# Kernel tuning notes

Hardware: AMD Instinct MI355X
Metric: run time of the kernel (lower is better)

Reference implementation:

```python
import jax, jax.numpy as jnp
import numpy as np

D_MODEL = 1024
N_HEADS = 16
D_FF = 4096
EPS = 1e-5


def setup_inputs() -> dict:
    key = jax.random.key(0)
    ks = jax.random.split(key, 16)
    s = 1.0 / np.sqrt(D_MODEL)
    x = jax.random.normal(ks[0], (4, 2048, D_MODEL), dtype=jnp.float32)
    Wq = jax.random.normal(ks[1], (D_MODEL, D_MODEL), jnp.float32) * s
    bq = jnp.zeros((D_MODEL,), jnp.float32)
    Wk = jax.random.normal(ks[2], (D_MODEL, D_MODEL), jnp.float32) * s
    bk = jnp.zeros((D_MODEL,), jnp.float32)
    Wv = jax.random.normal(ks[3], (D_MODEL, D_MODEL), jnp.float32) * s
    bv = jnp.zeros((D_MODEL,), jnp.float32)
    Wo = jax.random.normal(ks[4], (D_MODEL, D_MODEL), jnp.float32) * s
    bo = jnp.zeros((D_MODEL,), jnp.float32)
    W1 = jax.random.normal(ks[5], (D_MODEL, D_FF), jnp.float32) * s
    b1 = jnp.zeros((D_FF,), jnp.float32)
    W2 = jax.random.normal(ks[6], (D_FF, D_MODEL), jnp.float32) * (1.0 / np.sqrt(D_FF))
    b2 = jnp.zeros((D_MODEL,), jnp.float32)
    g1 = jnp.ones((D_MODEL,), jnp.float32)
    beta1 = jnp.zeros((D_MODEL,), jnp.float32)
    g2 = jnp.ones((D_MODEL,), jnp.float32)
    beta2 = jnp.zeros((D_MODEL,), jnp.float32)
    return {"x": x, "Wq": Wq, "bq": bq, "Wk": Wk, "bk": bk, "Wv": Wv, "bv": bv,
            "Wo": Wo, "bo": bo, "W1": W1, "b1": b1, "W2": W2, "b2": b2,
            "g1": g1, "beta1": beta1, "g2": g2, "beta2": beta2}


def _layernorm(x, g, b):
    mu = jnp.mean(x, axis=-1, keepdims=True)
    var = jnp.mean(jnp.square(x - mu), axis=-1, keepdims=True)
    return (x - mu) * jax.lax.rsqrt(var + EPS) * g + b


def reference(x, Wq, bq, Wk, bk, Wv, bv, Wo, bo, W1, b1, W2, b2, g1, beta1, g2, beta2):
    B, S, D = x.shape
    H, dk = N_HEADS, D // N_HEADS
    # QKV projections -> [B, H, S, dk]
    q = (x @ Wq + bq).reshape(B, S, H, dk).transpose(0, 2, 1, 3)
    k = (x @ Wk + bk).reshape(B, S, H, dk).transpose(0, 2, 1, 3)
    v = (x @ Wv + bv).reshape(B, S, H, dk).transpose(0, 2, 1, 3)
    scores = jnp.einsum('bhqd,bhkd->bhqk', q, k) / np.sqrt(dk)  # [B,H,S,S]
    attn = jax.nn.softmax(scores, axis=-1)
    out = jnp.einsum('bhqk,bhkd->bhqd', attn, v)
    out = out.transpose(0, 2, 1, 3).reshape(B, S, D) @ Wo + bo
    x2 = _layernorm(x + out, g1, beta1)
    ff = jax.nn.relu(x2 @ W1 + b1) @ W2 + b2
    return _layernorm(x2 + ff, g2, beta2)
```

## Files before the change

kernel.cpp:

```cpp
#include <hip/hip_runtime.h>
#include <math.h>
#include <stdint.h>


#define D_MODEL 1024
#define N_HEADS 16
#define DKH     64
#define D_FF    4096
#define BATCH   4
#define SEQ     2048
#define NTOK    (BATCH * SEQ)
#define LN_EPS  1e-5f
#define QKV_LD  3072
#define QSCALE  0.18033688011112042f

typedef unsigned short u16;
typedef __attribute__((ext_vector_type(8))) short bf16x8;
typedef __attribute__((ext_vector_type(4))) float f32x4;
typedef __attribute__((ext_vector_type(16))) float f32x16;

__device__ __forceinline__ u16 f2bf(float f) {
    union { float f; uint32_t u; } c; c.f = f;
    return (u16)((c.u + 0x7FFFu + ((c.u >> 16) & 1u)) >> 16);
}
__device__ __forceinline__ float bf2f(u16 h) {
    union { uint32_t u; float f; } c; c.u = ((uint32_t)h) << 16;
    return c.f;
}

__device__ __forceinline__ void gload16(const u16* g, u16* lds) {
    __builtin_amdgcn_global_load_lds(
        (const __attribute__((address_space(1))) uint32_t*)g,
        (__attribute__((address_space(3))) uint32_t*)(uintptr_t)lds,
        16, 0, 0);
}

__device__ __forceinline__ void store_out(float* p, float v) { *p = v; }
__device__ __forceinline__ void store_out(u16* p, float v)   { *p = f2bf(v); }

template <int MODE, typename OutT>
__global__ __launch_bounds__(512) void gemm_pipe_kernel(
    const u16* __restrict__ A, const u16* __restrict__ Bt,
    const float* __restrict__ bias, const float* __restrict__ bias2,
    const float* __restrict__ bias3, OutT* __restrict__ C,
    int M, int N, int K)
{
    __shared__ u16 lds[3 * 8192 + 2 * 16384];

    const int tid  = threadIdx.x;
    const int wave = tid >> 6;
    const int lane = tid & 63;
    const int lo   = lane & 15;
    const int hi   = lane >> 4;
    const int wr   = wave >> 2;
    const int wc   = wave & 3;

    const int gx  = gridDim.x;
    const int nwg = gx * gridDim.y;
    int bid = blockIdx.y * gx + blockIdx.x;
    bid = (bid & 7) * (nwg >> 3) + (bid >> 3);
    const int m0 = (bid / gx) << 7;
    const int n0 = (bid % gx) << 8;
    const int NT = K >> 6;

    const int srow = lane >> 3;
    const int schk = (lane & 7) ^ srow;
    const u16* AgS = A  + (size_t)(m0 + wave * 16 + srow) * K + schk * 8;
    const u16* BgS = Bt + (size_t)(n0 + wave * 32 + srow) * K + schk * 8;
    u16* AdS = lds + wave * 1024;
    u16* BdS = lds + 24576 + wave * 2048;

    auto stageA = [&](int kt, int buf) {
        const u16* g = AgS + kt * 64;
        u16* d = AdS + buf * 8192;
#pragma unroll
        for (int q = 0; q < 2; ++q)
            gload16(g + (size_t)q * 8 * K, d + q * 512);
    };
    auto stageB = [&](int kt, int buf) {
        const u16* g = BgS + kt * 64;
        u16* d = BdS + buf * 16384;
#pragma unroll
        for (int q = 0; q < 4; ++q)
            gload16(g + (size_t)q * 8 * K, d + q * 512);
    };

    f32x4 acc[4][4];
#pragma unroll
    for (int i = 0; i < 4; ++i)
#pragma unroll
        for (int j = 0; j < 4; ++j)
#pragma unroll
            for (int r = 0; r < 4; ++r) acc[i][j][r] = 0.f;

    stageA(0, 0);
    stageB(0, 0);
    stageA(1, 1);
    __builtin_amdgcn_sched_barrier(0);
    asm volatile("s_waitcnt vmcnt(2)" ::: "memory");
    __builtin_amdgcn_s_barrier();
    __builtin_amdgcn_sched_barrier(0);

    for (int t = 0; t < NT; ++t) {
        int tb = t + 1; if (tb >= NT) tb = 0;
        int ta = t + 2; if (ta >= NT) ta -= NT;
        stageB(tb, (t + 1) & 1);
        stageA(ta, (t + 2) % 3);

        const u16* Ab = lds + (t % 3) * 8192;
        const u16* Bb = lds + 24576 + (t & 1) * 16384;
#pragma unroll
        for (int ks = 0; ks < 2; ++ks) {
            bf16x8 a[4], b[4];
#pragma unroll
            for (int i = 0; i < 4; ++i) {
                const int ar = wr * 64 + i * 16 + lo;
                a[i] = *(const bf16x8*)&Ab[ar * 64 + (((ks * 4 + hi) ^ (ar & 7)) << 3)];
                const int br = wc * 64 + i * 16 + lo;
                b[i] = *(const bf16x8*)&Bb[br * 64 + (((ks * 4 + hi) ^ (br & 7)) << 3)];
            }
            __builtin_amdgcn_s_setprio(1);
#pragma unroll
            for (int i = 0; i < 4; ++i)
#pragma unroll
                for (int j = 0; j < 4; ++j)
                    acc[i][j] = __builtin_amdgcn_mfma_f32_16x16x32_bf16(
                                    a[i], b[j], acc[i][j], 0, 0, 0);
            __builtin_amdgcn_s_setprio(0);
        }
        __builtin_amdgcn_sched_barrier(0);
        asm volatile("s_waitcnt vmcnt(2)" ::: "memory");
        __builtin_amdgcn_s_barrier();
        __builtin_amdgcn_sched_barrier(0);
    }

    const int crow0 = m0 + wr * 64 + hi * 4;
    const int ccol0 = n0 + wc * 64 + lo;
#pragma unroll
    for (int j = 0; j < 4; ++j) {
        const int col = ccol0 + j * 16;
        float bj;
        float sc = 1.0f;
        if (MODE == 2) {
            bj = (col < 1024) ? bias[col]
               : (col < 2048) ? bias2[col - 1024] : bias3[col - 2048];
            if (col < 1024) sc = QSCALE;
        } else {
            bj = bias[col];
        }
#pragma unroll
        for (int i = 0; i < 4; ++i)
#pragma unroll
            for (int r = 0; r < 4; ++r) {
                float v = acc[i][j][r] + bj;
                if (MODE == 1) v = fmaxf(v, 0.f);
                if (MODE == 2) v *= sc;
                store_out(&C[(size_t)(crow0 + i * 16 + r) * N + col], v);
            }
    }
}

__global__ __launch_bounds__(256, 4) void attn_mfma_kernel(
    const u16* __restrict__ QKV, u16* __restrict__ O)
{
    __shared__ u16 Klds[2][64 * 64];
    __shared__ u16 Vlds[2][64 * 64];

    const int tid  = threadIdx.x;
    const int wave = tid >> 6;
    const int lane = tid & 63;
    const int l31  = lane & 31;
    const int hi5  = lane >> 5;
    const int b    = blockIdx.x >> 4;
    const int h    = blockIdx.x & 15;
    const int q0   = blockIdx.y * 128 + wave * 32;
    const size_t rowb = (size_t)b * SEQ * QKV_LD + (size_t)h * DKH;
    const u16* Qg = QKV + rowb;
    const u16* Kg = QKV + rowb + 1024;
    const u16* Vg = QKV + rowb + 2048;

    bf16x8 qf[4];
#pragma unroll
    for (int f = 0; f < 4; ++f)
        qf[f] = *(const bf16x8*)&Qg[(size_t)(q0 + l31) * QKV_LD + 16 * f + 8 * hi5];

    f32x16 oacc[2];
#pragma unroll
    for (int g = 0; g < 2; ++g)
#pragma unroll
        for (int r = 0; r < 16; ++r) oacc[g][r] = 0.f;
    float mrun = -1e30f, lrun = 0.f;

    const int krow = wave * 8 + (lane >> 3);
    const int kchk = ((lane & 7) ^ (lane >> 3)) << 3;

    const int vdk0 = (tid & 15) * 4;
    const int vkv  = (tid >> 4) * 4;
    const int vchk = vkv >> 3;
    const int vsub = vkv & 7;

    alignas(8) u16 e[4][4];

    auto stageK = [&](int kv0, int buf) {
        u16* kdst = &Klds[buf][wave * 512];
        gload16(Kg + (size_t)(kv0 + krow) * QKV_LD + kchk,      kdst);
        gload16(Kg + (size_t)(kv0 + krow + 32) * QKV_LD + kchk, kdst + 32 * 64);
    };
    auto loadV = [&](int kv0) {
#pragma unroll
        for (int i = 0; i < 4; ++i)
            *(uint2*)e[i] = *(const uint2*)&Vg[(size_t)(kv0 + vkv + i) * QKV_LD + vdk0];
    };
    auto writeV = [&](int buf) {
#pragma unroll
        for (int j = 0; j < 4; ++j) {
            alignas(8) u16 w4[4] = { e[0][j], e[1][j], e[2][j], e[3][j] };
            const int row = vdk0 + j;
            *(uint2*)&Vlds[buf][row * 64 + ((vchk ^ (row & 7)) << 3) + vsub] =
                *(const uint2*)w4;
        }
    };

    stageK(0, 0);
    loadV(0);
    writeV(0);
    __syncthreads();

    constexpr int NTILES = SEQ / 64;
    for (int t = 0; t < NTILES; ++t) {
        const int cur = t & 1, nxt = cur ^ 1;
        if (t + 1 < NTILES) {
            stageK((t + 1) * 64, nxt);
            loadV((t + 1) * 64);
        }

        f32x16 s0, s1;
#pragma unroll
        for (int r = 0; r < 16; ++r) { s0[r] = 0.f; s1[r] = 0.f; }
#pragma unroll
        for (int f = 0; f < 4; ++f) {
            const int rc = ((2 * f + hi5) ^ (l31 & 7)) << 3;
            const bf16x8 ka = *(const bf16x8*)&Klds[cur][l31 * 64 + rc];
            const bf16x8 kb = *(const bf16x8*)&Klds[cur][(32 + l31) * 64 + rc];
            s0 = __builtin_amdgcn_mfma_f32_32x32x16_bf16(ka, qf[f], s0, 0, 0, 0);
            s1 = __builtin_amdgcn_mfma_f32_32x32x16_bf16(kb, qf[f], s1, 0, 0, 0);
        }

        float mx[16];
#pragma unroll
        for (int r = 0; r < 16; ++r) mx[r] = fmaxf(s0[r], s1[r]);
#pragma unroll
        for (int off = 8; off >= 1; off >>= 1)
#pragma unroll
            for (int r = 0; r < off; ++r) mx[r] = fmaxf(mx[r], mx[r + off]);
        float tm = fmaxf(mx[0], __shfl_xor(mx[0], 32, 64));
        if (__any(tm > mrun + 8.0f)) {
            const float mnew = fmaxf(mrun, tm);
            const float corr = exp2f(mrun - mnew);
            lrun *= corr;
#pragma unroll
            for (int g = 0; g < 2; ++g)
#pragma unroll
                for (int r = 0; r < 16; ++r) oacc[g][r] *= corr;
            mrun = mnew;
        }
        float sm[16];
#pragma unroll
        for (int r = 0; r < 16; ++r) {
            s0[r] = exp2f(s0[r] - mrun);
            s1[r] = exp2f(s1[r] - mrun);
            sm[r] = s0[r] + s1[r];
        }
#pragma unroll
        for (int off = 8; off >= 1; off >>= 1)
#pragma unroll
            for (int r = 0; r < off; ++r) sm[r] += sm[r + off];
        lrun += sm[0];

        if (t + 1 < NTILES) writeV(nxt);

        auto mkfrag = [&](float a0, float a1, float a2, float a3,
                          float a4, float a5, float a6, float a7) -> bf16x8 {
            uint32_t A, B, C, D;
            asm("v_cvt_pk_bf16_f32 %0, %1, %2" : "=v"(A) : "v"(a0), "v"(a1));
            asm("v_cvt_pk_bf16_f32 %0, %1, %2" : "=v"(C) : "v"(a2), "v"(a3));
            asm("v_cvt_pk_bf16_f32 %0, %1, %2" : "=v"(B) : "v"(a4), "v"(a5));
            asm("v_cvt_pk_bf16_f32 %0, %1, %2" : "=v"(D) : "v"(a6), "v"(a7));
            asm volatile("v_permlane32_swap_b32 %0, %1" : "+v"(A), "+v"(B));
            asm volatile("v_permlane32_swap_b32 %0, %1" : "+v"(C), "+v"(D));
            union { uint32_t w[4]; bf16x8 v; } u;
            u.w[0] = A; u.w[1] = C; u.w[2] = B; u.w[3] = D;
            return u.v;
        };
        bf16x8 pb0 = mkfrag(s0[0], s0[1], s0[2],  s0[3],  s0[4],  s0[5],  s0[6],  s0[7]);
        bf16x8 pb1 = mkfrag(s0[8], s0[9], s0[10], s0[11], s0[12], s0[13], s0[14], s0[15]);
        bf16x8 pb2 = mkfrag(s1[0], s1[1], s1[2],  s1[3],  s1[4],  s1[5],  s1[6],  s1[7]);
        bf16x8 pb3 = mkfrag(s1[8], s1[9], s1[10], s1[11], s1[12], s1[13], s1[14], s1[15]);

#pragma unroll
        for (int f = 0; f < 4; ++f) {
            const bf16x8 pf = (f == 0) ? pb0 : (f == 1) ? pb1 : (f == 2) ? pb2 : pb3;
            const int rc = ((2 * f + hi5) ^ (l31 & 7)) << 3;
            const bf16x8 va = *(const bf16x8*)&Vlds[cur][l31 * 64 + rc];
            const bf16x8 vb = *(const bf16x8*)&Vlds[cur][(32 + l31) * 64 + rc];
            oacc[0] = __builtin_amdgcn_mfma_f32_32x32x16_bf16(va, pf, oacc[0], 0, 0, 0);
            oacc[1] = __builtin_amdgcn_mfma_f32_32x32x16_bf16(vb, pf, oacc[1], 0, 0, 0);
        }
        __syncthreads();
    }

    lrun += __shfl_xor(lrun, 32, 64);
    const float inv = 1.0f / lrun;
    u16* Orow = O + (size_t)b * SEQ * D_MODEL + (size_t)(q0 + l31) * D_MODEL + h * DKH;
#pragma unroll
    for (int g = 0; g < 2; ++g)
#pragma unroll
        for (int rp = 0; rp < 8; ++rp) {
            const int r = rp * 2;
            const float v0 = oacc[g][r] * inv;
            const float v1 = oacc[g][r + 1] * inv;
            uint32_t pk;
            asm("v_cvt_pk_bf16_f32 %0, %1, %2" : "=v"(pk) : "v"(v0), "v"(v1));
            const int d = 32 * g + (r & 3) + 8 * (r >> 2) + 4 * hi5;
            *(uint32_t*)&Orow[d] = pk;
        }
}

__global__ __launch_bounds__(256) void transpose_w_kernel(
    const float* __restrict__ W, u16* __restrict__ Wt, int K, int N)
{
    __shared__ float t[32][33];
    const int n0 = blockIdx.x << 5;
    const int k0 = blockIdx.y << 5;
    const int tx = threadIdx.x & 31;
    const int ty = threadIdx.x >> 5;
#pragma unroll
    for (int i = 0; i < 4; ++i)
        t[ty + i * 8][tx] = W[(size_t)(k0 + ty + i * 8) * N + n0 + tx];
    __syncthreads();
#pragma unroll
    for (int i = 0; i < 4; ++i)
        Wt[(size_t)(n0 + ty + i * 8) * K + k0 + tx] = f2bf(t[tx][ty + i * 8]);
}

__global__ __launch_bounds__(256) void cvt_kernel(
    const float* __restrict__ src, u16* __restrict__ dst)
{
    const size_t i = ((size_t)blockIdx.x * 256 + threadIdx.x) * 8;
    const float4 a = *(const float4*)&src[i];
    const float4 b = *(const float4*)&src[i + 4];
    alignas(16) u16 e[8] = { f2bf(a.x), f2bf(a.y), f2bf(a.z), f2bf(a.w),
                             f2bf(b.x), f2bf(b.y), f2bf(b.z), f2bf(b.w) };
    *(int4*)&dst[i] = *(const int4*)e;
}

__device__ __forceinline__ float4 ld4(const float* p) { return *(const float4*)p; }
__device__ __forceinline__ float4 ld4(const u16* p) {
    alignas(8) u16 e[4];
    *(uint2*)e = *(const uint2*)p;
    return make_float4(bf2f(e[0]), bf2f(e[1]), bf2f(e[2]), bf2f(e[3]));
}
__device__ __forceinline__ void st4(float* p, float4 v) { *(float4*)p = v; }
__device__ __forceinline__ void st4(u16* p, float4 v) {
    alignas(8) u16 e[4] = { f2bf(v.x), f2bf(v.y), f2bf(v.z), f2bf(v.w) };
    *(uint2*)p = *(const uint2*)e;
}

template <typename XT, typename YT, typename OT>
__global__ __launch_bounds__(256) void add_ln_kernel(
    const XT* __restrict__ X, const YT* __restrict__ Y,
    const float* __restrict__ gamma, const float* __restrict__ beta,
    OT* __restrict__ Out)
{
    const int row = blockIdx.x;
    const int i0  = threadIdx.x << 2;
    const float4 xv = ld4(X + (size_t)row * D_MODEL + i0);
    const float4 yv = ld4(Y + (size_t)row * D_MODEL + i0);
    const float4 v  = make_float4(xv.x + yv.x, xv.y + yv.y, xv.z + yv.z, xv.w + yv.w);

    float s1 = v.x + v.y + v.z + v.w;
    float s2 = v.x * v.x + v.y * v.y + v.z * v.z + v.w * v.w;
#pragma unroll
    for (int off = 32; off > 0; off >>= 1) {
        s1 += __shfl_xor(s1, off, 64);
        s2 += __shfl_xor(s2, off, 64);
    }
    __shared__ float red[8];
    const int wid = threadIdx.x >> 6;
    if ((threadIdx.x & 63) == 0) { red[wid] = s1; red[wid + 4] = s2; }
    __syncthreads();
    s1 = red[0] + red[1] + red[2] + red[3];
    s2 = red[4] + red[5] + red[6] + red[7];

    const float mu   = s1 * (1.0f / D_MODEL);
    const float var  = s2 * (1.0f / D_MODEL) - mu * mu;
    const float rstd = rsqrtf(var + LN_EPS);

    const float4 g  = *(const float4*)(gamma + i0);
    const float4 bb = *(const float4*)(beta + i0);
    float4 ov;
    ov.x = (v.x - mu) * rstd * g.x + bb.x;
    ov.y = (v.y - mu) * rstd * g.y + bb.y;
    ov.z = (v.z - mu) * rstd * g.z + bb.z;
    ov.w = (v.w - mu) * rstd * g.w + bb.w;
    st4(Out + (size_t)row * D_MODEL + i0, ov);
}

extern "C" void kernel_launch(void* const* d_in, const int* in_sizes, int n_in,
                              void* d_out, int out_size, void* d_ws, size_t ws_size,
                              hipStream_t stream)
{
    const float* x     = (const float*)d_in[0];
    const float* Wq    = (const float*)d_in[1];
    const float* bq    = (const float*)d_in[2];
    const float* Wk    = (const float*)d_in[3];
    const float* bk    = (const float*)d_in[4];
    const float* Wv    = (const float*)d_in[5];
    const float* bv    = (const float*)d_in[6];
    const float* Wo    = (const float*)d_in[7];
    const float* bo    = (const float*)d_in[8];
    const float* W1    = (const float*)d_in[9];
    const float* b1    = (const float*)d_in[10];
    const float* W2    = (const float*)d_in[11];
    const float* b2    = (const float*)d_in[12];
    const float* g1    = (const float*)d_in[13];
    const float* beta1 = (const float*)d_in[14];
    const float* g2    = (const float*)d_in[15];
    const float* beta2 = (const float*)d_in[16];
    float* out = (float*)d_out;

    const size_t TOKD = (size_t)NTOK * D_MODEL;
    u16* xb    = (u16*)d_ws;
    u16* wqkvT = xb + TOKD;
    u16* woT   = wqkvT + (size_t)3 * D_MODEL * D_MODEL;
    u16* w1T   = woT + (size_t)D_MODEL * D_MODEL;
    u16* w2T   = w1T + (size_t)D_MODEL * D_FF;
    u16* qkv   = w2T + (size_t)D_FF * D_MODEL;
    u16* ctx   = qkv + (size_t)NTOK * QKV_LD;
    u16* y1    = ctx + TOKD;
    u16* x2    = y1;
    u16* h1    = qkv;

    const dim3 blk(256);
    const dim3 blk5(512);

    cvt_kernel<<<dim3(TOKD / 2048), blk, 0, stream>>>(x, xb);
    transpose_w_kernel<<<dim3(D_MODEL / 32, D_MODEL / 32), blk, 0, stream>>>(Wq, wqkvT, D_MODEL, D_MODEL);
    transpose_w_kernel<<<dim3(D_MODEL / 32, D_MODEL / 32), blk, 0, stream>>>(Wk, wqkvT + (size_t)D_MODEL * D_MODEL, D_MODEL, D_MODEL);
    transpose_w_kernel<<<dim3(D_MODEL / 32, D_MODEL / 32), blk, 0, stream>>>(Wv, wqkvT + (size_t)2 * D_MODEL * D_MODEL, D_MODEL, D_MODEL);
    transpose_w_kernel<<<dim3(D_MODEL / 32, D_MODEL / 32), blk, 0, stream>>>(Wo, woT, D_MODEL, D_MODEL);
    transpose_w_kernel<<<dim3(D_FF / 32,    D_MODEL / 32), blk, 0, stream>>>(W1, w1T, D_MODEL, D_FF);
    transpose_w_kernel<<<dim3(D_MODEL / 32, D_FF / 32),    blk, 0, stream>>>(W2, w2T, D_FF, D_MODEL);

    gemm_pipe_kernel<2, u16><<<dim3(QKV_LD / 256, NTOK / 128), blk5, 0, stream>>>(
        xb, wqkvT, bq, bk, bv, qkv, NTOK, QKV_LD, D_MODEL);

    attn_mfma_kernel<<<dim3(BATCH * N_HEADS, SEQ / 128), blk, 0, stream>>>(qkv, ctx);

    gemm_pipe_kernel<0, u16><<<dim3(D_MODEL / 256, NTOK / 128), blk5, 0, stream>>>(
        ctx, woT, bo, bo, bo, y1, NTOK, D_MODEL, D_MODEL);

    add_ln_kernel<float, u16, u16><<<dim3(NTOK), blk, 0, stream>>>(x, y1, g1, beta1, x2);

    gemm_pipe_kernel<1, u16><<<dim3(D_FF / 256, NTOK / 128), blk5, 0, stream>>>(
        x2, w1T, b1, b1, b1, h1, NTOK, D_FF, D_MODEL);
    gemm_pipe_kernel<0, float><<<dim3(D_MODEL / 256, NTOK / 128), blk5, 0, stream>>>(
        h1, w2T, b2, b2, b2, out, NTOK, D_MODEL, D_FF);

    add_ln_kernel<u16, float, float><<<dim3(NTOK), blk, 0, stream>>>(x2, out, g2, beta2, out);

    (void)in_sizes; (void)n_in; (void)out_size; (void)ws_size;
}
```

Baseline: 407.7 us.

## Split GEMM k-loop into interleaved halves and compute softmax row sums via MFMA

The GEMM main loop is split into two k-halves, each issuing one global stage (B, then A) between LDS fragment reads and MFMAs, with extra workgroup barriers to interleave memory traffic with compute. In attention, the per-tile scalar row-sum reduction is dropped. The row sum is instead taken from an extra MFMA against a constant ones row placed in an enlarged V LDS buffer. V uses a new swizzle to reduce bank conflicts, and MFMA blocks get raised priority. The cost is more LDS, one third more PV MFMAs, and extra barriers in the GEMM.

```diff
diff --git a/kernel.cpp b/kernel.cpp
--- a/kernel.cpp
+++ b/kernel.cpp
@@ -104,30 +104,53 @@
     for (int t = 0; t < NT; ++t) {
         int tb = t + 1; if (tb >= NT) tb = 0;
         int ta = t + 2; if (ta >= NT) ta -= NT;
-        stageB(tb, (t + 1) & 1);
-        stageA(ta, (t + 2) % 3);
-
         const u16* Ab = lds + (t % 3) * 8192;
         const u16* Bb = lds + 24576 + (t & 1) * 16384;
-#pragma unroll
-        for (int ks = 0; ks < 2; ++ks) {
-            bf16x8 a[4], b[4];
-#pragma unroll
-            for (int i = 0; i < 4; ++i) {
-                const int ar = wr * 64 + i * 16 + lo;
-                a[i] = *(const bf16x8*)&Ab[ar * 64 + (((ks * 4 + hi) ^ (ar & 7)) << 3)];
-                const int br = wc * 64 + i * 16 + lo;
-                b[i] = *(const bf16x8*)&Bb[br * 64 + (((ks * 4 + hi) ^ (br & 7)) << 3)];
-            }
-            __builtin_amdgcn_s_setprio(1);
-#pragma unroll
-            for (int i = 0; i < 4; ++i)
-#pragma unroll
-                for (int j = 0; j < 4; ++j)
-                    acc[i][j] = __builtin_amdgcn_mfma_f32_16x16x32_bf16(
-                                    a[i], b[j], acc[i][j], 0, 0, 0);
-            __builtin_amdgcn_s_setprio(0);
-        }
+
+        bf16x8 a0[4], b0[4];
+#pragma unroll
+        for (int i = 0; i < 4; ++i) {
+            const int ar = wr * 64 + i * 16 + lo;
+            a0[i] = *(const bf16x8*)&Ab[ar * 64 + ((hi ^ (ar & 7)) << 3)];
+            const int br = wc * 64 + i * 16 + lo;
+            b0[i] = *(const bf16x8*)&Bb[br * 64 + ((hi ^ (br & 7)) << 3)];
+        }
+        stageB(tb, (t + 1) & 1);
+        __builtin_amdgcn_sched_barrier(0);
+        __builtin_amdgcn_s_barrier();
+        __builtin_amdgcn_sched_barrier(0);
+        __builtin_amdgcn_s_setprio(1);
+#pragma unroll
+        for (int i = 0; i < 4; ++i)
+#pragma unroll
+            for (int j = 0; j < 4; ++j)
+                acc[i][j] = __builtin_amdgcn_mfma_f32_16x16x32_bf16(
+                                a0[i], b0[j], acc[i][j], 0, 0, 0);
+        __builtin_amdgcn_s_setprio(0);
+        __builtin_amdgcn_sched_barrier(0);
+        __builtin_amdgcn_s_barrier();
+        __builtin_amdgcn_sched_barrier(0);
+
+        bf16x8 a1[4], b1[4];
+#pragma unroll
+        for (int i = 0; i < 4; ++i) {
+            const int ar = wr * 64 + i * 16 + lo;
+            a1[i] = *(const bf16x8*)&Ab[ar * 64 + (((4 + hi) ^ (ar & 7)) << 3)];
+            const int br = wc * 64 + i * 16 + lo;
+            b1[i] = *(const bf16x8*)&Bb[br * 64 + (((4 + hi) ^ (br & 7)) << 3)];
+        }
+        stageA(ta, (t + 2) % 3);
+        __builtin_amdgcn_sched_barrier(0);
+        __builtin_amdgcn_s_barrier();
+        __builtin_amdgcn_sched_barrier(0);
+        __builtin_amdgcn_s_setprio(1);
+#pragma unroll
+        for (int i = 0; i < 4; ++i)
+#pragma unroll
+            for (int j = 0; j < 4; ++j)
+                acc[i][j] = __builtin_amdgcn_mfma_f32_16x16x32_bf16(
+                                a1[i], b1[j], acc[i][j], 0, 0, 0);
+        __builtin_amdgcn_s_setprio(0);
         __builtin_amdgcn_sched_barrier(0);
         asm volatile("s_waitcnt vmcnt(2)" ::: "memory");
         __builtin_amdgcn_s_barrier();
@@ -164,7 +187,7 @@
     const u16* __restrict__ QKV, u16* __restrict__ O)
 {
     __shared__ u16 Klds[2][64 * 64];
-    __shared__ u16 Vlds[2][64 * 64];
+    __shared__ u16 Vlds[2][96 * 64];
 
     const int tid  = threadIdx.x;
     const int wave = tid >> 6;
@@ -179,17 +202,29 @@
     const u16* Kg = QKV + rowb + 1024;
     const u16* Vg = QKV + rowb + 2048;
 
+    {
+        const int ibuf = tid >> 7;
+        const int irow = 64 + ((tid >> 2) & 31);
+        const uint32_t ival = (irow == 64) ? 0x3F803F80u : 0u;
+        const uint4 iv = make_uint4(ival, ival, ival, ival);
+        *(uint4*)&Vlds[ibuf][irow * 64 + (tid & 3) * 16]     = iv;
+        *(uint4*)&Vlds[ibuf][irow * 64 + (tid & 3) * 16 + 8] = iv;
+    }
+
     bf16x8 qf[4];
 #pragma unroll
     for (int f = 0; f < 4; ++f)
         qf[f] = *(const bf16x8*)&Qg[(size_t)(q0 + l31) * QKV_LD + 16 * f + 8 * hi5];
 
     f32x16 oacc[2];
+    f32x16 oacc2;
 #pragma unroll
     for (int g = 0; g < 2; ++g)
 #pragma unroll
         for (int r = 0; r < 16; ++r) oacc[g][r] = 0.f;
-    float mrun = -1e30f, lrun = 0.f;
+#pragma unroll
+    for (int r = 0; r < 16; ++r) oacc2[r] = 0.f;
+    float mrun = -1e30f;
 
     const int krow = wave * 8 + (lane >> 3);
     const int kchk = ((lane & 7) ^ (lane >> 3)) << 3;
@@ -198,6 +233,9 @@
     const int vkv  = (tid >> 4) * 4;
     const int vchk = vkv >> 3;
     const int vsub = vkv & 7;
+
+    const int ha = (l31 ^ (l31 >> 3)) & 7;
+    const int hb = ha ^ 4;
 
     alignas(8) u16 e[4][4];
 
@@ -216,7 +254,8 @@
         for (int j = 0; j < 4; ++j) {
             alignas(8) u16 w4[4] = { e[0][j], e[1][j], e[2][j], e[3][j] };
             const int row = vdk0 + j;
-            *(uint2*)&Vlds[buf][row * 64 + ((vchk ^ (row & 7)) << 3) + vsub] =
+            const int hsh = (row ^ (row >> 3)) & 7;
+            *(uint2*)&Vlds[buf][row * 64 + ((vchk ^ hsh) << 3) + vsub] =
                 *(const uint2*)w4;
         }
     };
@@ -237,6 +276,7 @@
         f32x16 s0, s1;
 #pragma unroll
         for (int r = 0; r < 16; ++r) { s0[r] = 0.f; s1[r] = 0.f; }
+        __builtin_amdgcn_s_setprio(1);
 #pragma unroll
         for (int f = 0; f < 4; ++f) {
             const int rc = ((2 * f + hi5) ^ (l31 & 7)) << 3;
@@ -245,6 +285,7 @@
             s0 = __builtin_amdgcn_mfma_f32_32x32x16_bf16(ka, qf[f], s0, 0, 0, 0);
             s1 = __builtin_amdgcn_mfma_f32_32x32x16_bf16(kb, qf[f], s1, 0, 0, 0);
         }
+        __builtin_amdgcn_s_setprio(0);
 
         float mx[16];
 #pragma unroll
@@ -257,25 +298,18 @@
         if (__any(tm > mrun + 8.0f)) {
             const float mnew = fmaxf(mrun, tm);
             const float corr = exp2f(mrun - mnew);
-            lrun *= corr;
 #pragma unroll
             for (int g = 0; g < 2; ++g)
 #pragma unroll
                 for (int r = 0; r < 16; ++r) oacc[g][r] *= corr;
+            oacc2[0] *= corr;
             mrun = mnew;
         }
-        float sm[16];
 #pragma unroll
         for (int r = 0; r < 16; ++r) {
             s0[r] = exp2f(s0[r] - mrun);
             s1[r] = exp2f(s1[r] - mrun);
-            sm[r] = s0[r] + s1[r];
-        }
-#pragma unroll
-        for (int off = 8; off >= 1; off >>= 1)
-#pragma unroll
-            for (int r = 0; r < off; ++r) sm[r] += sm[r + off];
-        lrun += sm[0];
+        }
 
         if (t + 1 < NTILES) writeV(nxt);
 
@@ -297,20 +331,26 @@
         bf16x8 pb2 = mkfrag(s1[0], s1[1], s1[2],  s1[3],  s1[4],  s1[5],  s1[6],  s1[7]);
         bf16x8 pb3 = mkfrag(s1[8], s1[9], s1[10], s1[11], s1[12], s1[13], s1[14], s1[15]);
 
+        __builtin_amdgcn_s_setprio(1);
 #pragma unroll
         for (int f = 0; f < 4; ++f) {
             const bf16x8 pf = (f == 0) ? pb0 : (f == 1) ? pb1 : (f == 2) ? pb2 : pb3;
-            const int rc = ((2 * f + hi5) ^ (l31 & 7)) << 3;
-            const bf16x8 va = *(const bf16x8*)&Vlds[cur][l31 * 64 + rc];
-            const bf16x8 vb = *(const bf16x8*)&Vlds[cur][(32 + l31) * 64 + rc];
+            const int ca = ((2 * f + hi5) ^ ha) << 3;
+            const int cb = ((2 * f + hi5) ^ hb) << 3;
+            const bf16x8 va = *(const bf16x8*)&Vlds[cur][l31 * 64 + ca];
+            const bf16x8 vb = *(const bf16x8*)&Vlds[cur][(32 + l31) * 64 + cb];
+            const bf16x8 vc = *(const bf16x8*)&Vlds[cur][(64 + l31) * 64 + ca];
             oacc[0] = __builtin_amdgcn_mfma_f32_32x32x16_bf16(va, pf, oacc[0], 0, 0, 0);
             oacc[1] = __builtin_amdgcn_mfma_f32_32x32x16_bf16(vb, pf, oacc[1], 0, 0, 0);
-        }
+            oacc2   = __builtin_amdgcn_mfma_f32_32x32x16_bf16(vc, pf, oacc2,   0, 0, 0);
+        }
+        __builtin_amdgcn_s_setprio(0);
         __syncthreads();
     }
 
-    lrun += __shfl_xor(lrun, 32, 64);
-    const float inv = 1.0f / lrun;
+    float lr = oacc2[0];
+    lr += __shfl_xor(lr, 32, 64);
+    const float inv = 1.0f / lr;
     u16* Orow = O + (size_t)b * SEQ * D_MODEL + (size_t)(q0 + l31) * D_MODEL + h * DKH;
 #pragma unroll
     for (int g = 0; g < 2; ++g)
```

New measurement: 443.7 us. 8.8% more time.

## Single-buffer attention K/V tiles, new V swizzle, raise priority around MFMAs

Applied to the files above, without the earlier changes.

Drops the double-buffered K/V staging in the attention kernel in favour of one LDS buffer per tile, loaded at the top of each iteration between two barriers. The V tile gets a new XOR swizzle that mixes in higher row bits, intended to reduce bank conflicts when writing the transpose. The MFMA sections are wrapped in s_setprio. The aim is to halve LDS use and rely on occupancy across workgroups instead of intra-block prefetch, at the cost of no longer overlapping global loads with compute within a block.

```diff
diff --git a/kernel.cpp b/kernel.cpp
--- a/kernel.cpp
+++ b/kernel.cpp
@@ -163,8 +163,8 @@
 __global__ __launch_bounds__(256, 4) void attn_mfma_kernel(
     const u16* __restrict__ QKV, u16* __restrict__ O)
 {
-    __shared__ u16 Klds[2][64 * 64];
-    __shared__ u16 Vlds[2][64 * 64];
+    __shared__ u16 Klds[64 * 64];
+    __shared__ u16 Vlds[64 * 64];
 
     const int tid  = threadIdx.x;
     const int wave = tid >> 6;
@@ -193,58 +193,46 @@
 
     const int krow = wave * 8 + (lane >> 3);
     const int kchk = ((lane & 7) ^ (lane >> 3)) << 3;
+    u16* kdst = Klds + wave * 512;
 
     const int vdk0 = (tid & 15) * 4;
     const int vkv  = (tid >> 4) * 4;
     const int vchk = vkv >> 3;
     const int vsub = vkv & 7;
 
-    alignas(8) u16 e[4][4];
-
-    auto stageK = [&](int kv0, int buf) {
-        u16* kdst = &Klds[buf][wave * 512];
+    const int ha = (l31 ^ (l31 >> 3)) & 7;
+    const int hb = ha ^ 4;
+
+    for (int kv0 = 0; kv0 < SEQ; kv0 += 64) {
+        __syncthreads();
         gload16(Kg + (size_t)(kv0 + krow) * QKV_LD + kchk,      kdst);
         gload16(Kg + (size_t)(kv0 + krow + 32) * QKV_LD + kchk, kdst + 32 * 64);
-    };
-    auto loadV = [&](int kv0) {
+        alignas(8) u16 e[4][4];
 #pragma unroll
         for (int i = 0; i < 4; ++i)
             *(uint2*)e[i] = *(const uint2*)&Vg[(size_t)(kv0 + vkv + i) * QKV_LD + vdk0];
-    };
-    auto writeV = [&](int buf) {
 #pragma unroll
         for (int j = 0; j < 4; ++j) {
             alignas(8) u16 w4[4] = { e[0][j], e[1][j], e[2][j], e[3][j] };
             const int row = vdk0 + j;
-            *(uint2*)&Vlds[buf][row * 64 + ((vchk ^ (row & 7)) << 3) + vsub] =
-                *(const uint2*)w4;
-        }
-    };
-
-    stageK(0, 0);
-    loadV(0);
-    writeV(0);
-    __syncthreads();
-
-    constexpr int NTILES = SEQ / 64;
-    for (int t = 0; t < NTILES; ++t) {
-        const int cur = t & 1, nxt = cur ^ 1;
-        if (t + 1 < NTILES) {
-            stageK((t + 1) * 64, nxt);
-            loadV((t + 1) * 64);
-        }
+            const int hsh = (row ^ (row >> 3)) & 7;
+            *(uint2*)&Vlds[row * 64 + ((vchk ^ hsh) << 3) + vsub] = *(const uint2*)w4;
+        }
+        __syncthreads();
 
         f32x16 s0, s1;
 #pragma unroll
         for (int r = 0; r < 16; ++r) { s0[r] = 0.f; s1[r] = 0.f; }
+        __builtin_amdgcn_s_setprio(1);
 #pragma unroll
         for (int f = 0; f < 4; ++f) {
             const int rc = ((2 * f + hi5) ^ (l31 & 7)) << 3;
-            const bf16x8 ka = *(const bf16x8*)&Klds[cur][l31 * 64 + rc];
-            const bf16x8 kb = *(const bf16x8*)&Klds[cur][(32 + l31) * 64 + rc];
+            const bf16x8 ka = *(const bf16x8*)&Klds[l31 * 64 + rc];
+            const bf16x8 kb = *(const bf16x8*)&Klds[(32 + l31) * 64 + rc];
             s0 = __builtin_amdgcn_mfma_f32_32x32x16_bf16(ka, qf[f], s0, 0, 0, 0);
             s1 = __builtin_amdgcn_mfma_f32_32x32x16_bf16(kb, qf[f], s1, 0, 0, 0);
         }
+        __builtin_amdgcn_s_setprio(0);
 
         float mx[16];
 #pragma unroll
@@ -276,8 +264,6 @@
 #pragma unroll
             for (int r = 0; r < off; ++r) sm[r] += sm[r + off];
         lrun += sm[0];
-
-        if (t + 1 < NTILES) writeV(nxt);
 
         auto mkfrag = [&](float a0, float a1, float a2, float a3,
                           float a4, float a5, float a6, float a7) -> bf16x8 {
@@ -297,16 +283,18 @@
         bf16x8 pb2 = mkfrag(s1[0], s1[1], s1[2],  s1[3],  s1[4],  s1[5],  s1[6],  s1[7]);
         bf16x8 pb3 = mkfrag(s1[8], s1[9], s1[10], s1[11], s1[12], s1[13], s1[14], s1[15]);
 
+        __builtin_amdgcn_s_setprio(1);
 #pragma unroll
         for (int f = 0; f < 4; ++f) {
             const bf16x8 pf = (f == 0) ? pb0 : (f == 1) ? pb1 : (f == 2) ? pb2 : pb3;
-            const int rc = ((2 * f + hi5) ^ (l31 & 7)) << 3;
-            const bf16x8 va = *(const bf16x8*)&Vlds[cur][l31 * 64 + rc];
-            const bf16x8 vb = *(const bf16x8*)&Vlds[cur][(32 + l31) * 64 + rc];
+            const int ca = ((2 * f + hi5) ^ ha) << 3;
+            const int cb = ((2 * f + hi5) ^ hb) << 3;
+            const bf16x8 va = *(const bf16x8*)&Vlds[l31 * 64 + ca];
+            const bf16x8 vb = *(const bf16x8*)&Vlds[(32 + l31) * 64 + cb];
             oacc[0] = __builtin_amdgcn_mfma_f32_32x32x16_bf16(va, pf, oacc[0], 0, 0, 0);
             oacc[1] = __builtin_amdgcn_mfma_f32_32x32x16_bf16(vb, pf, oacc[1], 0, 0, 0);
         }
-        __syncthreads();
+        __builtin_amdgcn_s_setprio(0);
     }
 
     lrun += __shfl_xor(lrun, 32, 64);
```

Result: faster. 393.8 us (-3.4%).
